# Performance work log

Hardware: AMD Instinct MI355X
Metric: run time of the kernel (lower is better)

The kernel has to match this reference:

```python
import jax, jax.numpy as jnp
import numpy as np

EPS_PD = 1e-6    # torch F.pairwise_distance eps (added to x - y before norm)
EPS_NORM = 1e-12  # torch F.normalize eps


def l2_normalize(x):
    n = jnp.sqrt(jnp.sum(x * x, axis=1, keepdims=True))
    return x / jnp.maximum(n, EPS_NORM)


def pairwise_l2(x, y):
    # Faithful to ||x_i - y_j + eps||_2 (torch pairwise_distance adds scalar eps
    # to every coordinate of the difference) but computed via Gram matrices
    D = x.shape[1]
    xx = jnp.sum(x * x, axis=1)            # [B]
    yy = jnp.sum(y * y, axis=1)            # [B]
    xy = x @ y.T                           # [B, B]
    sq = xx[:, None] + yy[None, :] - 2.0 * xy
    # cross terms from the +eps shift: 2*eps*sum(x_i - y_j) + D*eps^2
    sq = sq + 2.0 * EPS_PD * (jnp.sum(x, axis=1)[:, None] - jnp.sum(y, axis=1)[None, :])
    sq = sq + D * (EPS_PD * EPS_PD)
    return jnp.sqrt(jnp.maximum(sq, 0.0))


def setup_inputs() -> dict:
    key = jax.random.key(0)
    k1, k2 = jax.random.split(key)
    B, D = 4096, 512
    low_feature = jax.random.normal(k1, (B, D), dtype=jnp.float32)
    embed_feature = jax.random.normal(k2, (B, D), dtype=jnp.float32)
    id_numpy = jnp.arange(B, dtype=jnp.int64 if jax.config.read('jax_enable_x64') else jnp.int32).reshape(B, 1)
    return {"low_feature": low_feature, "embed_feature": embed_feature, "id_numpy": id_numpy}


def reference(low_feature, embed_feature, id_numpy):
    # ids are unique (arange), so the set()-dedup in the original is identity.
    B = low_feature.shape[0]
    K = B  # k_num == current_batch_size -> x_start = y_start = 0

    low_n = l2_normalize(low_feature)
    emb_n = l2_normalize(embed_feature)

    dist_low = pairwise_l2(low_n, low_n)      # [B, B]
    dist_embed = pairwise_l2(emb_n, emb_n)    # [B, B]

    dl1 = dist_low[: K - 1, : K - 2]
    dl2 = dist_low[: K - 1, 1 : K - 1]
    de1 = dist_embed[: K - 1, : K - 2]
    de2 = dist_embed[: K - 1, 1 : K - 1]

    coeff = jnp.sign(dl1 - dl2) - jnp.sign(de1 - de2)
    dist_embed_inverse = de2 - de1
    loss_structure = jnp.mean(coeff * dist_embed_inverse)
    return loss_structure
```

## Files before the change

### kernel.cpp

```cpp
#include <hip/hip_runtime.h>
#include <hip/hip_bf16.h>
#include <hip/hip_fp8.h>
#include <math.h>

#define BROWS 4096
#define DIM   512
#define YEMB_B 2097152
#define TSTRIDE 191
#define NT 22

typedef float f32x4 __attribute__((ext_vector_type(4)));

__global__ __launch_bounds__(256) void prep4_kernel(
    const float* __restrict__ low, const float* __restrict__ emb,
    unsigned char* __restrict__ Yq,
    float* __restrict__ s_l, float* __restrict__ r_l,
    float* __restrict__ s_e, float* __restrict__ r_e,
    float* __restrict__ out) {
  const int tid = threadIdx.x;
  const int lane = tid & 63, wid = tid >> 6;
  const int rid = blockIdx.x * 4 + wid;
  if (blockIdx.x == 0 && tid == 0) out[0] = 0.f;

  const bool is_low = (rid < BROWS);
  const int row = is_low ? rid : rid - BROWS;
  const float* x = (is_low ? low : emb) + (size_t)row * DIM;

  const float4 v0 = ((const float4*)x)[lane * 2];
  const float4 v1 = ((const float4*)x)[lane * 2 + 1];

  float ss = v0.x * v0.x + v0.y * v0.y + v0.z * v0.z + v0.w * v0.w +
             v1.x * v1.x + v1.y * v1.y + v1.z * v1.z + v1.w * v1.w;
#pragma unroll
  for (int o = 1; o < 64; o <<= 1) ss += __shfl_xor(ss, o, 64);
  const float inv = 1.0f / fmaxf(sqrtf(ss), 1e-12f);

  float y[8] = {v0.x * inv, v0.y * inv, v0.z * inv, v0.w * inv,
                v1.x * inv, v1.y * inv, v1.z * inv, v1.w * inv};

  union { unsigned char b[8]; unsigned long long u; } pk;
  float sv = 0.f, rv = 0.f;
#pragma unroll
  for (int i = 0; i < 8; ++i) {
    pk.b[i] = __hip_fp8_e4m3(y[i]).__x;
    sv += y[i] * y[i];
    rv += y[i];
  }
  ((unsigned long long*)(Yq + (size_t)rid * 512))[lane] = pk.u;

#pragma unroll
  for (int o = 1; o < 64; o <<= 1) {
    sv += __shfl_xor(sv, o, 64);
    rv += __shfl_xor(rv, o, 64);
  }
  if (lane == 0) {
    (is_low ? s_l : s_e)[row] = sv;
    (is_low ? r_l : r_e)[row] = rv;
  }
}

__global__ __launch_bounds__(512, 2) void fused_sym_kernel(
    const unsigned char* __restrict__ Yq,
    const float* __restrict__ s_l, const float* __restrict__ r_l,
    const float* __restrict__ s_e, const float* __restrict__ r_e,
    float* __restrict__ out) {
  __shared__ __align__(16) unsigned char lds8[98304];
  __shared__ float hand_d[4][48][2];
  __shared__ float hand_t[4][192][2];
  __shared__ float sred[8];

  int rem = blockIdx.x, br = 0;
  while (rem >= NT - br) { rem -= NT - br; ++br; }
  const int bc = br + rem;
  const bool diag = (br == bc);

  const int tid = threadIdx.x;
  const int lane = tid & 63;
  const int wid = tid >> 6;
  const int wr = wid >> 1;
  const int wc = wid & 1;
  const int quad = lane >> 4, cpos = lane & 15;
  const int r0 = br * TSTRIDE, c0 = bc * TSTRIDE;

  int goff[6];
#pragma unroll
  for (int s = 0; s < 6; ++s) {
    const int c = tid + 512 * s;
    const int seg = c / 768;
    const int within = c - seg * 768;
    const int rp = within >> 3;
    const int cc = within & 7;
    const int rloc = 2 * rp + (cc >> 2);
    const int gch = (cc & 3) ^ (rp & 3);
    int base;
    if (seg == 0)      base = min(r0 + rloc, BROWS - 1) * 512;
    else if (seg == 1) base = YEMB_B + min(r0 + rloc, BROWS - 1) * 512;
    else if (seg == 2) base = min(c0 + rloc, BROWS - 1) * 512;
    else               base = YEMB_B + min(c0 + rloc, BROWS - 1) * 512;
    goff[s] = base + (gch << 4);
  }

  auto STAGE = [&](int t, int b) {
    const int k0 = t * 64;
#pragma unroll
    for (int s = 0; s < 6; ++s) {
      if (s < 3 || !diag)
        __builtin_amdgcn_global_load_lds(
            (const __attribute__((address_space(1))) void*)(Yq + goff[s] + k0),
            (__attribute__((address_space(3))) void*)(lds8 + b * 49152 +
                                                      (tid + 512 * s) * 16),
            16, 0, 0);
    }
  };

  const int RaH = (48 * wr + cpos) >> 1;
  const int s3a = RaH & 3;
  const int aoff = RaH * 128 + (cpos & 1) * 64 + (quad & 1) * 8;
  const int RbH = (96 * wc + cpos) >> 1;
  const int s3b = RbH & 3;
  const int boff = RbH * 128 + (cpos & 1) * 64 + (quad & 1) * 8;
  const int segAL = 0, segAE = 12288;
  const int segBL = diag ? 0 : 24576;
  const int segBE = diag ? 12288 : 36864;

  f32x4 accl[3][6], acce[3][6];
#pragma unroll
  for (int u = 0; u < 3; ++u)
#pragma unroll
    for (int v = 0; v < 6; ++v) {
      accl[u][v] = (f32x4)(0.f);
      acce[u][v] = (f32x4)(0.f);
    }

  STAGE(0, 0);

  for (int t = 0; t < 8; ++t) {
    if (t < 7) STAGE(t + 1, (t + 1) & 1);
    if (t == 7)      asm volatile("s_waitcnt vmcnt(0)" ::: "memory");
    else if (diag)   asm volatile("s_waitcnt vmcnt(3)" ::: "memory");
    else             asm volatile("s_waitcnt vmcnt(6)" ::: "memory");
    __builtin_amdgcn_s_barrier();
    __builtin_amdgcn_sched_barrier(0);

    const unsigned char* Lb = lds8 + (t & 1) * 49152;
#pragma unroll
    for (int kk = 0; kk < 2; ++kk) {
      const int q = 2 * kk + (quad >> 1);
      const int cha = aoff + ((q ^ s3a) << 4);
      const int chb = boff + ((q ^ s3b) << 4);
      {
        long a[3], b[6];
#pragma unroll
        for (int u = 0; u < 3; ++u) a[u] = *(const long*)(Lb + segAL + cha + u * 1024);
#pragma unroll
        for (int v = 0; v < 6; ++v) b[v] = *(const long*)(Lb + segBL + chb + v * 1024);
        __builtin_amdgcn_s_setprio(1);
#pragma unroll
        for (int u = 0; u < 3; ++u)
#pragma unroll
          for (int v = 0; v < 6; ++v)
            accl[u][v] = __builtin_amdgcn_mfma_f32_16x16x32_fp8_fp8(
                a[u], b[v], accl[u][v], 0, 0, 0);
        __builtin_amdgcn_s_setprio(0);
      }
      {
        long a[3], b[6];
#pragma unroll
        for (int u = 0; u < 3; ++u) a[u] = *(const long*)(Lb + segAE + cha + u * 1024);
#pragma unroll
        for (int v = 0; v < 6; ++v) b[v] = *(const long*)(Lb + segBE + chb + v * 1024);
        __builtin_amdgcn_s_setprio(1);
#pragma unroll
        for (int u = 0; u < 3; ++u)
#pragma unroll
          for (int v = 0; v < 6; ++v)
            acce[u][v] = __builtin_amdgcn_mfma_f32_16x16x32_fp8_fp8(
                a[u], b[v], acce[u][v], 0, 0, 0);
        __builtin_amdgcn_s_setprio(0);
      }
    }
    __builtin_amdgcn_sched_barrier(0);
    __builtin_amdgcn_s_barrier();
    __builtin_amdgcn_sched_barrier(0);
  }

  const float epst = (float)DIM * 1e-6f * 1e-6f;
#pragma unroll
  for (int v = 0; v < 6; ++v) {
    const int j = min(c0 + 96 * wc + 16 * v + cpos, BROWS - 1);
    const float sjl = s_l[j], rjl = r_l[j];
    const float sje = s_e[j], rje = r_e[j];
#pragma unroll
    for (int u = 0; u < 3; ++u)
#pragma unroll
      for (int r = 0; r < 4; ++r) {
        const int i = min(r0 + 48 * wr + 16 * u + 4 * quad + r, BROWS - 1);
        const float sql = s_l[i] + sjl - 2.f * accl[u][v][r] +
                          2e-6f * (r_l[i] - rjl) + epst;
        accl[u][v][r] = sqrtf(fmaxf(sql, 0.f));
        const float sqe = s_e[i] + sje - 2.f * acce[u][v][r] +
                          2e-6f * (r_e[i] - rje) + epst;
        acce[u][v][r] = sqrtf(fmaxf(sqe, 0.f));
      }
  }

  if (wc == 1 && cpos == 0) {
#pragma unroll
    for (int u = 0; u < 3; ++u)
#pragma unroll
      for (int r = 0; r < 4; ++r) {
        hand_d[wr][16 * u + 4 * quad + r][0] = accl[u][0][r];
        hand_d[wr][16 * u + 4 * quad + r][1] = acce[u][0][r];
      }
  }
  if (quad == 0 && wr >= 1) {
#pragma unroll
    for (int v = 0; v < 6; ++v) {
      hand_t[wr - 1][96 * wc + 16 * v + cpos][0] = accl[0][v][0];
      hand_t[wr - 1][96 * wc + 16 * v + cpos][1] = acce[0][v][0];
    }
  }
  __syncthreads();

  float sum = 0.f;

  const int srcin = (lane & 48) | ((cpos + 1) & 15);
#pragma unroll
  for (int u = 0; u < 3; ++u)
#pragma unroll
    for (int r = 0; r < 4; ++r) {
      const int trow = 48 * wr + 16 * u + 4 * quad + r;
      const int i = r0 + trow;
      const bool rowok = (trow <= TSTRIDE - 1) && (i <= BROWS - 2);
#pragma unroll
      for (int v = 0; v < 6; ++v) {
        const float dl1 = accl[u][v][r], de1 = acce[u][v][r];
        float dl2 = __shfl(dl1, srcin, 64);
        float de2 = __shfl(de1, srcin, 64);
        if (v < 5) {
          const float dlb = __shfl(accl[u][v + 1][r], lane & 48, 64);
          const float deb = __shfl(acce[u][v + 1][r], lane & 48, 64);
          if (cpos == 15) { dl2 = dlb; de2 = deb; }
        } else if (cpos == 15 && wc == 0) {
          dl2 = hand_d[wr][16 * u + 4 * quad + r][0];
          de2 = hand_d[wr][16 * u + 4 * quad + r][1];
        }
        const int tcol = 96 * wc + 16 * v + cpos;
        const int j = c0 + tcol;
        if (rowok && tcol <= TSTRIDE - 1 && j <= BROWS - 3) {
          const float aa = dl1 - dl2, bb = de1 - de2;
          const float coeff = (float)((aa > 0.f) - (aa < 0.f)) -
                              (float)((bb > 0.f) - (bb < 0.f));
          sum += coeff * (de2 - de1);
        }
      }
    }

  if (!diag) {
#pragma unroll
    for (int u = 0; u < 3; ++u)
#pragma unroll
      for (int v = 0; v < 6; ++v) {
        const int tcol = 96 * wc + 16 * v + cpos;
        const int ii = c0 + tcol;
        const bool colok = (tcol <= TSTRIDE - 1) && (ii <= BROWS - 2);
#pragma unroll
        for (int r = 0; r < 4; ++r) {
          const int trow = 48 * wr + 16 * u + 4 * quad + r;
          const int jj = r0 + trow;
          float dl2, de2;
          if (r < 3) {
            dl2 = accl[u][v][r + 1];
            de2 = acce[u][v][r + 1];
          } else {
            const float dlq = __shfl(accl[u][v][0], (lane + 16) & 63, 64);
            const float deq = __shfl(acce[u][v][0], (lane + 16) & 63, 64);
            const int un = (u < 2) ? u + 1 : u;
            const float dlu = __shfl(accl[un][v][0], cpos, 64);
            const float deu = __shfl(acce[un][v][0], cpos, 64);
            if (quad < 3)    { dl2 = dlq; de2 = deq; }
            else if (u < 2)  { dl2 = dlu; de2 = deu; }
            else             { dl2 = hand_t[wr][tcol][0];
                               de2 = hand_t[wr][tcol][1]; }
          }
          if (colok && trow <= TSTRIDE - 1 && jj <= BROWS - 3) {
            const float dl1 = accl[u][v][r], de1 = acce[u][v][r];
            const float aa = dl1 - dl2, bb = de1 - de2;
            const float coeff = (float)((aa > 0.f) - (aa < 0.f)) -
                                (float)((bb > 0.f) - (bb < 0.f));
            sum += coeff * (de2 - de1);
          }
        }
      }
  }

#pragma unroll
  for (int o = 32; o; o >>= 1) sum += __shfl_down(sum, o, 64);
  if (lane == 0) sred[wid] = sum;
  __syncthreads();
  if (tid == 0) {
    const float scale = 1.0f / ((float)(BROWS - 1) * (float)(BROWS - 2));
    float t = 0.f;
#pragma unroll
    for (int w = 0; w < 8; ++w) t += sred[w];
    atomicAdd(out, t * scale);
  }
}

extern "C" void kernel_launch(void* const* d_in, const int* in_sizes, int n_in,
                              void* d_out, int out_size, void* d_ws,
                              size_t ws_size, hipStream_t stream) {
  const float* low = (const float*)d_in[0];
  const float* emb = (const float*)d_in[1];
  float* out = (float*)d_out;

  unsigned char* Yq = (unsigned char*)d_ws;
  float* s_l = (float*)(Yq + 2 * (size_t)BROWS * DIM);
  float* r_l = s_l + BROWS;
  float* s_e = r_l + BROWS;
  float* r_e = s_e + BROWS;

  prep4_kernel<<<2 * BROWS / 4, 256, 0, stream>>>(low, emb, Yq, s_l, r_l, s_e, r_e, out);
  fused_sym_kernel<<<NT * (NT + 1) / 2, 512, 0, stream>>>(Yq, s_l, r_l, s_e, r_e, out);
}
```

Baseline: 108.4 us.

## Load A fragments directly from global into registers, stage only B in LDS

The A-side operand fragments (row tile) are now read straight from global memory into registers, double-buffered across k-steps, and only the B-side (column tile) goes through LDS via global_load_lds. This halves the LDS footprint and the LDS read traffic for A, which may allow more occupancy and cut LDS bank pressure. The cost is more VGPRs for the register double buffer, uncoalesced 8-byte global loads for A that depend on L2 hits, and a fixed vmcnt(15) wait that must match the exact count of outstanding loads.

```diff
diff --git a/kernel.cpp b/kernel.cpp
--- a/kernel.cpp
+++ b/kernel.cpp
@@ -64,7 +64,7 @@
     const float* __restrict__ s_l, const float* __restrict__ r_l,
     const float* __restrict__ s_e, const float* __restrict__ r_e,
     float* __restrict__ out) {
-  __shared__ __align__(16) unsigned char lds8[98304];
+  __shared__ __align__(16) unsigned char lds8[49152];
   __shared__ float hand_d[4][48][2];
   __shared__ float hand_t[4][192][2];
   __shared__ float sred[8];
@@ -82,9 +82,9 @@
   const int quad = lane >> 4, cpos = lane & 15;
   const int r0 = br * TSTRIDE, c0 = bc * TSTRIDE;
 
-  int goff[6];
-#pragma unroll
-  for (int s = 0; s < 6; ++s) {
+  int goff[3];
+#pragma unroll
+  for (int s = 0; s < 3; ++s) {
     const int c = tid + 512 * s;
     const int seg = c / 768;
     const int within = c - seg * 768;
@@ -92,36 +92,41 @@
     const int cc = within & 7;
     const int rloc = 2 * rp + (cc >> 2);
     const int gch = (cc & 3) ^ (rp & 3);
-    int base;
-    if (seg == 0)      base = min(r0 + rloc, BROWS - 1) * 512;
-    else if (seg == 1) base = YEMB_B + min(r0 + rloc, BROWS - 1) * 512;
-    else if (seg == 2) base = min(c0 + rloc, BROWS - 1) * 512;
-    else               base = YEMB_B + min(c0 + rloc, BROWS - 1) * 512;
+    const int base = (seg ? YEMB_B : 0) + min(c0 + rloc, BROWS - 1) * 512;
     goff[s] = base + (gch << 4);
   }
 
   auto STAGE = [&](int t, int b) {
     const int k0 = t * 64;
 #pragma unroll
-    for (int s = 0; s < 6; ++s) {
-      if (s < 3 || !diag)
-        __builtin_amdgcn_global_load_lds(
-            (const __attribute__((address_space(1))) void*)(Yq + goff[s] + k0),
-            (__attribute__((address_space(3))) void*)(lds8 + b * 49152 +
-                                                      (tid + 512 * s) * 16),
-            16, 0, 0);
-    }
+    for (int s = 0; s < 3; ++s)
+      __builtin_amdgcn_global_load_lds(
+          (const __attribute__((address_space(1))) void*)(Yq + goff[s] + k0),
+          (__attribute__((address_space(3))) void*)(lds8 + b * 24576 +
+                                                    (tid + 512 * s) * 16),
+          16, 0, 0);
   };
 
-  const int RaH = (48 * wr + cpos) >> 1;
-  const int s3a = RaH & 3;
-  const int aoff = RaH * 128 + (cpos & 1) * 64 + (quad & 1) * 8;
+  int aoffg[3];
+#pragma unroll
+  for (int u = 0; u < 3; ++u)
+    aoffg[u] = min(r0 + 48 * wr + 16 * u + cpos, BROWS - 1) * 512 +
+               (quad >> 1) * 16 + (quad & 1) * 8;
+
+  auto ALOAD = [&](int t, long (&aL)[6], long (&aE)[6]) {
+#pragma unroll
+    for (int u = 0; u < 3; ++u)
+#pragma unroll
+      for (int kk = 0; kk < 2; ++kk) {
+        const int o = aoffg[u] + t * 64 + kk * 32;
+        aL[u * 2 + kk] = *(const long*)(Yq + o);
+        aE[u * 2 + kk] = *(const long*)(Yq + YEMB_B + o);
+      }
+  };
+
   const int RbH = (96 * wc + cpos) >> 1;
   const int s3b = RbH & 3;
   const int boff = RbH * 128 + (cpos & 1) * 64 + (quad & 1) * 8;
-  const int segAL = 0, segAE = 12288;
-  const int segBL = diag ? 0 : 24576;
-  const int segBE = diag ? 12288 : 36864;
 
   f32x4 accl[3][6], acce[3][6];
 #pragma unroll
@@ -132,56 +137,63 @@
       acce[u][v] = (f32x4)(0.f);
     }
 
+  long aL0[6], aE0[6], aL1[6], aE1[6];
   STAGE(0, 0);
-
-  for (int t = 0; t < 8; ++t) {
-    if (t < 7) STAGE(t + 1, (t + 1) & 1);
-    if (t == 7)      asm volatile("s_waitcnt vmcnt(0)" ::: "memory");
-    else if (diag)   asm volatile("s_waitcnt vmcnt(3)" ::: "memory");
-    else             asm volatile("s_waitcnt vmcnt(6)" ::: "memory");
+  ALOAD(0, aL0, aE0);
+
+  auto ROUND = [&](int t, long (&aLc)[6], long (&aEc)[6],
+                   long (&aLn)[6], long (&aEn)[6]) {
+    if (t < 7) {
+      STAGE(t + 1, (t + 1) & 1);
+      ALOAD(t + 1, aLn, aEn);
+    }
+    if (t == 7) asm volatile("s_waitcnt vmcnt(0)" ::: "memory");
+    else        asm volatile("s_waitcnt vmcnt(15)" ::: "memory");
     __builtin_amdgcn_s_barrier();
     __builtin_amdgcn_sched_barrier(0);
 
-    const unsigned char* Lb = lds8 + (t & 1) * 49152;
+    const unsigned char* Lb = lds8 + (t & 1) * 24576;
 #pragma unroll
     for (int kk = 0; kk < 2; ++kk) {
       const int q = 2 * kk + (quad >> 1);
-      const int cha = aoff + ((q ^ s3a) << 4);
       const int chb = boff + ((q ^ s3b) << 4);
       {
-        long a[3], b[6];
-#pragma unroll
-        for (int u = 0; u < 3; ++u) a[u] = *(const long*)(Lb + segAL + cha + u * 1024);
-#pragma unroll
-        for (int v = 0; v < 6; ++v) b[v] = *(const long*)(Lb + segBL + chb + v * 1024);
+        long b[6];
+#pragma unroll
+        for (int v = 0; v < 6; ++v) b[v] = *(const long*)(Lb + chb + v * 1024);
         __builtin_amdgcn_s_setprio(1);
 #pragma unroll
         for (int u = 0; u < 3; ++u)
 #pragma unroll
           for (int v = 0; v < 6; ++v)
             accl[u][v] = __builtin_amdgcn_mfma_f32_16x16x32_fp8_fp8(
-                a[u], b[v], accl[u][v], 0, 0, 0);
+                aLc[u * 2 + kk], b[v], accl[u][v], 0, 0, 0);
         __builtin_amdgcn_s_setprio(0);
       }
       {
-        long a[3], b[6];
-#pragma unroll
-        for (int u = 0; u < 3; ++u) a[u] = *(const long*)(Lb + segAE + cha + u * 1024);
-#pragma unroll
-        for (int v = 0; v < 6; ++v) b[v] = *(const long*)(Lb + segBE + chb + v * 1024);
+        long b[6];
+#pragma unroll
+        for (int v = 0; v < 6; ++v)
+          b[v] = *(const long*)(Lb + 12288 + chb + v * 1024);
         __builtin_amdgcn_s_setprio(1);
 #pragma unroll
         for (int u = 0; u < 3; ++u)
 #pragma unroll
           for (int v = 0; v < 6; ++v)
             acce[u][v] = __builtin_amdgcn_mfma_f32_16x16x32_fp8_fp8(
-                a[u], b[v], acce[u][v], 0, 0, 0);
+                aEc[u * 2 + kk], b[v], acce[u][v], 0, 0, 0);
         __builtin_amdgcn_s_setprio(0);
       }
     }
     __builtin_amdgcn_sched_barrier(0);
     __builtin_amdgcn_s_barrier();
     __builtin_amdgcn_sched_barrier(0);
+  };
+
+#pragma unroll
+  for (int tt = 0; tt < 4; ++tt) {
+    ROUND(2 * tt,     aL0, aE0, aL1, aE1);
+    ROUND(2 * tt + 1, aL1, aE1, aL0, aE0);
   }
 
   const float epst = (float)DIM * 1e-6f * 1e-6f;
```

Result: slower. 121.9 us (+12.5%).
